# Optimization experiments

Hardware: AMD Instinct MI355X
Metric: run time of the kernel (lower is better)

## Reference

```python
import jax, jax.numpy as jnp
import numpy as np

B, N, DEG, F_IN, D = 32, 1024, 16, 8, 64

def setup_inputs() -> dict:
    key = jax.random.key(0)
    ks = jax.random.split(key, 24)
    T = B * N
    E = B * N * DEG
    x = jax.random.normal(ks[0], (T, F_IN), dtype=jnp.float32)
    # edges confined within each graph (block-diagonal batched graph)
    off = (jnp.arange(B) * N)[:, None]
    src = jax.random.randint(ks[1], (B, N * DEG), 0, N) + off
    dst = jax.random.randint(ks[2], (B, N * DEG), 0, N) + off
    edge_index = jnp.stack([src.reshape(-1), dst.reshape(-1)]).astype(jnp.int64)
    reachable = jax.random.randint(ks[3], (T,), 0, 2, dtype=jnp.int32)
    s = 0.1
    p = lambda k, shp: jax.random.normal(k, shp, dtype=jnp.float32) * s
    return {
        'x': x, 'edge_index': edge_index, 'reachable': reachable,
        'Wl0': p(ks[4], (D, F_IN)), 'Wr0': p(ks[5], (D, F_IN)),
        'att0': p(ks[6], (D,)), 'b0': p(ks[7], (D,)),
        'Wl': p(ks[8], (4, D, D)), 'Wr': p(ks[9], (4, D, D)),
        'att': p(ks[10], (4, D)), 'b': p(ks[11], (4, D)),
        't6w': p(ks[12], (D, D)), 't6b': p(ks[13], (D,)),
        't7w': p(ks[14], (D, D)), 't7b': p(ks[15], (D,)),
        't5pw': p(ks[16], (1, 2 * D)), 't5pb': p(ks[17], (1,)),
        't5vw': p(ks[18], (1, 2 * D)), 't5vb': p(ks[19], (1,)),
        'pw': p(ks[20], (1, 1)), 'pb': p(ks[21], (1,)),
        'vw': p(ks[22], (1, 1)), 'vb': p(ks[23], (1,)),
        'n_per_graph': N,
    }

def reference(x, edge_index, reachable, Wl0, Wr0, att0, b0, Wl, Wr, att, b,
              t6w, t6b, t7w, t7b, t5pw, t5pb, t5vw, t5vb, pw, pb, vw, vb,
              n_per_graph):
    T = x.shape[0]
    n = int(n_per_graph)
    bsz = T // n
    d = Wl0.shape[0]
    # GATv2Conv adds self loops by default
    loop = jnp.arange(T)
    src = jnp.concatenate([edge_index[0], loop])
    dst = jnp.concatenate([edge_index[1], loop])

    def gatv2(h, WlK, WrK, a, bb):
        xl = h @ WlK.T                                  # [T, d]
        xr = h @ WrK.T
        e = jax.nn.leaky_relu(xl[src] + xr[dst], 0.2) @ a  # [E]
        emax = jax.ops.segment_max(e, dst, num_segments=T)
        ee = jnp.exp(e - emax[dst])
        denom = jax.ops.segment_sum(ee, dst, num_segments=T)
        alpha = ee / denom[dst]                         # edge softmax per target
        return jax.ops.segment_sum(alpha[:, None] * xl[src], dst, num_segments=T) + bb

    h = gatv2(x, Wl0, Wr0, att0, b0)
    for k in range(Wl.shape[0]):  # ReLU between layers, none after last
        h = gatv2(jax.nn.relu(h), Wl[k], Wr[k], att[k], b[k])
    mu_raw = h                                          # [T, d]

    # scatter_mean pooling per graph + repeat_interleave back to nodes
    mu_mp = mu_raw.reshape(bsz, n, d).mean(axis=1)      # [B, d]
    mu_mp_exp = jnp.repeat(mu_mp, n, axis=0)            # [T, d]

    g = mu_mp_exp @ t6w.T + t6b
    l = mu_raw @ t7w.T + t7b
    rep = jax.nn.relu(jnp.concatenate([g, l], axis=1))  # [T, 2d]

    prob_logits = rep @ t5pw.T + t5pb                   # [T, 1]
    logits = (prob_logits * pw[0, 0] + pb[0]).reshape(bsz, n, 1)

    q = (rep @ t5vw.T + t5vb)[:, 0]                     # [T]
    q = jnp.where(reachable.astype(bool), q, jnp.float32(-1e20))
    v = q.reshape(bsz, n).max(axis=1, keepdims=True)    # [B, 1]
    value = v * vw[0, 0] + vb[0]
    return logits, value
```

## Files before the change

kernel.cpp:

```cpp
#include <hip/hip_runtime.h>
#include <hip/hip_bf16.h>

typedef unsigned short u16;

#define T_NODES 32768
#define NPG 1024
#define BGR 32
#define D 64
#define FIN 8
#define SLOTS 64

typedef __attribute__((ext_vector_type(8))) short short8v;
typedef __attribute__((ext_vector_type(4))) float floatx4;
typedef __attribute__((ext_vector_type(2))) float f32x2;

__device__ __forceinline__ float bf2f(u16 u){ return __uint_as_float(((unsigned)u) << 16); }
__device__ __forceinline__ u16 f2bf(float f){
    __hip_bfloat16 h = __float2bfloat16(f);
    return *reinterpret_cast<u16*>(&h);
}
__device__ __forceinline__ f32x2 lo_hi(unsigned w){
    f32x2 r;
    r[0] = __uint_as_float(w << 16);
    r[1] = __uint_as_float(w & 0xffff0000u);
    return r;
}
__device__ __forceinline__ f32x2 lrelu2(f32x2 v){
    return __builtin_elementwise_max(v, v * 0.2f);
}
__device__ __forceinline__ short8v pack_bf8(float4 a, float4 b){
    short8v r;
    r[0]=(short)f2bf(a.x); r[1]=(short)f2bf(a.y);
    r[2]=(short)f2bf(a.z); r[3]=(short)f2bf(a.w);
    r[4]=(short)f2bf(b.x); r[5]=(short)f2bf(b.y);
    r[6]=(short)f2bf(b.z); r[7]=(short)f2bf(b.w);
    return r;
}

__device__ __forceinline__ unsigned fenc(float f){
    unsigned b = __float_as_uint(f);
    return (b & 0x80000000u) ? ~b : (b | 0x80000000u);
}
__device__ __forceinline__ float fdec(unsigned k){
    unsigned b = (k & 0x80000000u) ? (k ^ 0x80000000u) : ~k;
    return __uint_as_float(b);
}

template<int CTRL, int RM, int BM>
__device__ __forceinline__ float dpp_add(float x){
    int y = __builtin_amdgcn_update_dpp(0, __float_as_int(x), CTRL, RM, BM, false);
    return x + __int_as_float(y);
}
__device__ __forceinline__ float wave_sum63(float x){
    x = dpp_add<0x111,0xf,0xf>(x);
    x = dpp_add<0x112,0xf,0xf>(x);
    x = dpp_add<0x114,0xf,0xe>(x);
    x = dpp_add<0x118,0xf,0xc>(x);
    x = dpp_add<0x142,0xa,0xf>(x);
    x = dpp_add<0x143,0xc,0xf>(x);
    return x;
}
__device__ __forceinline__ float wave_sum_bcast(float x){
    return __int_as_float(__builtin_amdgcn_readlane(__float_as_int(wave_sum63(x)), 63));
}
__device__ __forceinline__ float row_ror_add(float x){
    x = dpp_add<0x121,0xf,0xf>(x);
    x = dpp_add<0x122,0xf,0xf>(x);
    x = dpp_add<0x124,0xf,0xf>(x);
    x = dpp_add<0x128,0xf,0xf>(x);
    return x;
}

__device__ __forceinline__ void edge_body(uint2 uv, bool valid,
        f32x2 a01, f32x2 a23, f32x2 xr01, f32x2 xr23,
        f32x2& acc01, f32x2& acc23, float& l){
    f32x2 x01 = lo_hi(uv.x);
    f32x2 x23 = lo_hi(uv.y);
    f32x2 v01 = lrelu2(x01 + xr01);
    f32x2 v23 = lrelu2(x23 + xr23);
    f32x2 e2 = v01 * a01 + v23 * a23;
    float e = e2[0] + e2[1];
    e = row_ror_add(e);
    float q = valid ? __expf(e) : 0.f;
    acc01 += q * x01;
    acc23 += q * x23;
    l += q;
}

__device__ __forceinline__ void node_edge(const u16* __restrict__ xlin,
        const int* colSh, int eb, int t, int deg, int sub4,
        f32x2 a01, f32x2 a23, f32x2 xr01, f32x2 xr23,
        f32x2& acc01, f32x2& acc23, float& l){
    int nEdge = deg + 1;
    for (int j0 = 0; j0 < nEdge; j0 += 8){
        uint2 u[8];
        #pragma unroll
        for (int i = 0; i < 8; i++){
            int j = j0 + i;
            int jc = (j < nEdge) ? j : (nEdge-1);
            int s = (jc < deg) ? colSh[eb + jc] : t;
            u[i] = *(const uint2*)&xlin[((size_t)(unsigned)s << 6) + sub4];
        }
        #pragma unroll
        for (int i = 0; i < 8; i++)
            edge_body(u[i], j0 + i < nEdge, a01, a23, xr01, xr23, acc01, acc23, l);
    }
}

__global__ void countscat_kernel(const int* __restrict__ src, const int* __restrict__ dst,
                                 int* __restrict__ counts, int* __restrict__ col64, int E){
    int i = blockIdx.x*blockDim.x + threadIdx.x;
    if (i < E){
        int d = dst[i];
        int slot = atomicAdd(&counts[d], 1);
        if (slot < SLOTS) col64[((size_t)d << 6) + slot] = src[i];
    }
}

__global__ void lin0_kernel(const float* __restrict__ x, const float* __restrict__ Wl0,
                            const float* __restrict__ Wr0,
                            u16* __restrict__ xlb, u16* __restrict__ xrb,
                            int* __restrict__ counts, float* __restrict__ muAcc,
                            unsigned* __restrict__ vslot, int* __restrict__ done,
                            int* __restrict__ pgdone, int* __restrict__ pgflag){
    __shared__ float wl[D][FIN+1];
    __shared__ float wr[D][FIN+1];
    __shared__ float xs[32][FIN];
    int tid = threadIdx.x;
    int blk = blockIdx.x;
    int gidx = blk*256 + tid;
    if (gidx < T_NODES) counts[gidx] = 0;
    if (gidx < BGR*D)   muAcc[gidx] = 0.f;
    if (gidx < BGR){ vslot[gidx] = 0u; done[gidx] = 0; pgdone[gidx] = 0; pgflag[gidx] = 0; }
    int rowBase = (blk & 7)*4096 + (blk >> 3)*32;
    for (int i = tid; i < D*FIN; i += 256){
        wl[i>>3][i&7] = Wl0[i];
        wr[i>>3][i&7] = Wr0[i];
    }
    xs[tid>>3][tid&7] = x[rowBase*FIN + tid];
    __syncthreads();
    int wave = tid >> 6, lane = tid & 63;
    int rb = rowBase + wave*8;
    #pragma unroll
    for (int r = 0; r < 8; r++){
        float al = 0.f, ar = 0.f;
        int lr = wave*8 + r;
        #pragma unroll
        for (int k = 0; k < FIN; k++){
            float xv = xs[lr][k];
            al = fmaf(xv, wl[lane][k], al);
            ar = fmaf(xv, wr[lane][k], ar);
        }
        xlb[(size_t)(rb+r)*D + lane] = f2bf(al);
        xrb[(size_t)(rb+r)*D + lane] = f2bf(ar);
    }
}

__global__ __launch_bounds__(256) void el_kernel(
        const u16* __restrict__ xlin, const u16* __restrict__ xrin,
        const float* __restrict__ att, const float* __restrict__ bias,
        const int* __restrict__ counts, const int* __restrict__ col64,
        const float* __restrict__ Wl, const float* __restrict__ Wr,
        u16* __restrict__ xlout, u16* __restrict__ xrout){
    __shared__ __align__(16) u16 hs[16][80];
    __shared__ __align__(16) int colSh[16*SLOTS];
    __shared__ int cnt[16];
    int tid = threadIdx.x, blk = blockIdx.x;
    int rowBase = (blk & 7)*4096 + (blk >> 3)*16;
    if (tid < 16){
        int c = counts[rowBase + tid];
        cnt[tid] = c < SLOTS ? c : SLOTS;
    }
    *(int4*)&colSh[tid*4] = *(const int4*)&col64[((size_t)rowBase << 6) + tid*4];
    __syncthreads();
    int wave = tid >> 6, lane = tid & 63;
    int g = lane >> 4, sub4 = (lane & 15) << 2;
    int ln = wave*4 + g;
    int t  = rowBase + ln;
    f32x2 a01 = { att[sub4],   att[sub4+1] };
    f32x2 a23 = { att[sub4+2], att[sub4+3] };
    float4 b4 = *(const float4*)&bias[sub4];
    uint2 xru = *(const uint2*)&xrin[((size_t)t << 6) + sub4];
    f32x2 xr01 = lo_hi(xru.x), xr23 = lo_hi(xru.y);
    int deg = cnt[ln];
    f32x2 acc01 = {0.f,0.f}, acc23 = {0.f,0.f};
    float l = 0.f;
    node_edge(xlin, colSh, ln*SLOTS, t, deg, sub4,
              a01, a23, xr01, xr23, acc01, acc23, l);
    float rl = __frcp_rn(l);
    ushort4 hb;
    hb.x = f2bf(fmaxf(fmaf(acc01[0], rl, b4.x), 0.f));
    hb.y = f2bf(fmaxf(fmaf(acc01[1], rl, b4.y), 0.f));
    hb.z = f2bf(fmaxf(fmaf(acc23[0], rl, b4.z), 0.f));
    hb.w = f2bf(fmaxf(fmaf(acc23[1], rl, b4.w), 0.f));
    *(ushort4*)&hs[ln][sub4] = hb;
    int lw = lane & 15, lg = lane >> 4, kb = lg*8;
    int colw = (wave << 4) + lw;
    const float* wl0 = &Wl[colw*D + kb];
    const float* wr0 = &Wr[colw*D + kb];
    short8v bl0 = pack_bf8(*(const float4*)wl0,        *(const float4*)(wl0+4));
    short8v bl1 = pack_bf8(*(const float4*)(wl0+32),   *(const float4*)(wl0+36));
    short8v br0 = pack_bf8(*(const float4*)wr0,        *(const float4*)(wr0+4));
    short8v br1 = pack_bf8(*(const float4*)(wr0+32),   *(const float4*)(wr0+36));
    __syncthreads();
    short8v a0 = *(const short8v*)&hs[lw][kb];
    short8v a1 = *(const short8v*)&hs[lw][32 + kb];
    floatx4 cl = {0.f,0.f,0.f,0.f}, cr = {0.f,0.f,0.f,0.f};
    cl = __builtin_amdgcn_mfma_f32_16x16x32_bf16(a0, bl0, cl, 0, 0, 0);
    cl = __builtin_amdgcn_mfma_f32_16x16x32_bf16(a1, bl1, cl, 0, 0, 0);
    cr = __builtin_amdgcn_mfma_f32_16x16x32_bf16(a0, br0, cr, 0, 0, 0);
    cr = __builtin_amdgcn_mfma_f32_16x16x32_bf16(a1, br1, cr, 0, 0, 0);
    size_t rb = (size_t)(rowBase + lg*4);
    #pragma unroll
    for (int j = 0; j < 4; j++){
        xlout[(rb + j)*D + colw] = f2bf(cl[j]);
        xrout[(rb + j)*D + colw] = f2bf(cr[j]);
    }
}

__global__ __launch_bounds__(256) void e4final_kernel(
        const u16* __restrict__ xlin, const u16* __restrict__ xrin,
        const float* __restrict__ att, const float* __restrict__ bias,
        const int* __restrict__ counts, const int* __restrict__ col64,
        const float* __restrict__ t6w, const float* __restrict__ t6b,
        const float* __restrict__ t7w, const float* __restrict__ t7b,
        const float* __restrict__ t5pw, const float* __restrict__ t5pb,
        const float* __restrict__ t5vw, const float* __restrict__ t5vb,
        const float* __restrict__ pw, const float* __restrict__ pb,
        const float* __restrict__ vw, const float* __restrict__ vb,
        const int* __restrict__ reachable,
        float* __restrict__ muAcc, unsigned* __restrict__ vslot,
        int* __restrict__ done, int* __restrict__ pgdone,
        int* __restrict__ pgflag, float* __restrict__ gPQ,
        float* __restrict__ out_logits, float* __restrict__ out_value){
    __shared__ __align__(16) char arena[43776];
    __shared__ float muS[D];
    __shared__ float PgQgS[2];
    __shared__ int isLastS;
    float* hfin  = (float*)arena;
    int*   colSh = (int*)  (arena + 17408);
    int*   cnt   = (int*)  (arena + 33792);
    float* wsH   = (float*)(arena + 17408);
    float* ppar  = (float*)(arena + 34816);
    float* qpar  = (float*)(arena + 39168);

    int tid = threadIdx.x, blk = blockIdx.x;
    int rowBase = (blk & 7)*4096 + (blk >> 3)*64;
    int b = rowBase >> 10;
    if (tid < 64){
        int c = counts[rowBase + tid];
        cnt[tid] = c < SLOTS ? c : SLOTS;
    }
    for (int i = tid; i < 1024; i += 256)
        *(int4*)&colSh[i*4] = *(const int4*)&col64[((size_t)rowBase << 6) + i*4];
    __syncthreads();
    int wave = tid >> 6, lane = tid & 63;
    int g = lane >> 4, sub4 = (lane & 15) << 2;
    int gid = wave*4 + g;
    f32x2 a01 = { att[sub4],   att[sub4+1] };
    f32x2 a23 = { att[sub4+2], att[sub4+3] };
    float4 b4 = *(const float4*)&bias[sub4];
    for (int n = 0; n < 4; n++){
        int ln = gid + n*16;
        int t  = rowBase + ln;
        uint2 xru = *(const uint2*)&xrin[((size_t)t << 6) + sub4];
        f32x2 xr01 = lo_hi(xru.x), xr23 = lo_hi(xru.y);
        int deg = cnt[ln];
        f32x2 acc01 = {0.f,0.f}, acc23 = {0.f,0.f};
        float l = 0.f;
        node_edge(xlin, colSh, ln*SLOTS, t, deg, sub4,
                  a01, a23, xr01, xr23, acc01, acc23, l);
        float rl = __frcp_rn(l);
        float4 hv;
        hv.x = fmaf(acc01[0], rl, b4.x);
        hv.y = fmaf(acc01[1], rl, b4.y);
        hv.z = fmaf(acc23[0], rl, b4.z);
        hv.w = fmaf(acc23[1], rl, b4.w);
        *(float4*)&hfin[ln*68 + sub4] = hv;
    }
    __syncthreads();
    for (int i = tid; i < D*D; i += 256) wsH[(i>>6)*68 + (i&63)] = t7w[i];
    if (wave == 0){
        float s = 0.f;
        #pragma unroll
        for (int nn = 0; nn < 64; nn++) s += hfin[nn*68 + lane];
        atomicAdd(&muAcc[b*D + lane], s);
    }
    __syncthreads();
    if (tid == 0){
        int tk = atomicAdd(&pgdone[b], 1);
        isLastS = (tk == (NPG/64) - 1);
    }
    __syncthreads();
    if (isLastS){
        if (tid < D)
            muS[tid] = __hip_atomic_load(&muAcc[b*D + tid], __ATOMIC_RELAXED,
                                         __HIP_MEMORY_SCOPE_AGENT) * (1.f/NPG);
        __syncthreads();
        if (tid < D){
            int d = tid;
            float gg = t6b[d];
            #pragma unroll
            for (int k = 0; k < D; k++) gg = fmaf(muS[k], t6w[d*D + k], gg);
            gg = fmaxf(gg, 0.f);
            float pp = wave_sum_bcast(gg * t5pw[d]);
            float qq = wave_sum_bcast(gg * t5vw[d]);
            if (d == 0){
                __hip_atomic_store(&gPQ[b*2],   pp, __ATOMIC_RELAXED, __HIP_MEMORY_SCOPE_AGENT);
                __hip_atomic_store(&gPQ[b*2+1], qq, __ATOMIC_RELAXED, __HIP_MEMORY_SCOPE_AGENT);
                asm volatile("s_waitcnt vmcnt(0)" ::: "memory");
                __hip_atomic_store(&pgflag[b], 1, __ATOMIC_RELAXED, __HIP_MEMORY_SCOPE_AGENT);
            }
        }
    }
    int ty = tid >> 4, tx = tid & 15;
    int r0 = ty * 4;
    float acc[4][4];
    #pragma unroll
    for (int i = 0; i < 4; i++)
        #pragma unroll
        for (int j = 0; j < 4; j++) acc[i][j] = 0.f;
    for (int k = 0; k < D; k += 4){
        float4 hv[4], wv[4];
        #pragma unroll
        for (int i = 0; i < 4; i++){
            hv[i] = *(const float4*)&hfin[(r0+i)*68 + k];
            wv[i] = *(const float4*)&wsH[(tx + 16*i)*68 + k];
        }
        #pragma unroll
        for (int i = 0; i < 4; i++)
            #pragma unroll
            for (int j = 0; j < 4; j++)
                acc[i][j] += hv[i].x*wv[j].x + hv[i].y*wv[j].y
                           + hv[i].z*wv[j].z + hv[i].w*wv[j].w;
    }
    float bc[4], pwc[4], qwc[4];
    #pragma unroll
    for (int j = 0; j < 4; j++){
        int c = tx + 16*j;
        bc[j]  = t7b[c];
        pwc[j] = t5pw[D + c];
        qwc[j] = t5vw[D + c];
    }
    #pragma unroll
    for (int i = 0; i < 4; i++){
        float sp = 0.f, sq = 0.f;
        #pragma unroll
        for (int j = 0; j < 4; j++){
            float lv = fmaxf(acc[i][j] + bc[j], 0.f);
            sp = fmaf(lv, pwc[j], sp);
            sq = fmaf(lv, qwc[j], sq);
        }
        ppar[(r0+i)*17 + tx] = sp;
        qpar[(r0+i)*17 + tx] = sq;
    }
    __syncthreads();
    if (tid == 0){
        while (__hip_atomic_load(&pgflag[b], __ATOMIC_RELAXED,
                                 __HIP_MEMORY_SCOPE_AGENT) == 0)
            __builtin_amdgcn_s_sleep(16);
        PgQgS[0] = __hip_atomic_load(&gPQ[b*2],   __ATOMIC_RELAXED, __HIP_MEMORY_SCOPE_AGENT);
        PgQgS[1] = __hip_atomic_load(&gPQ[b*2+1], __ATOMIC_RELAXED, __HIP_MEMORY_SCOPE_AGENT);
    }
    __syncthreads();
    if (tid < 64){
        int t = rowBase + tid;
        float sp = 0.f, sq = 0.f;
        #pragma unroll
        for (int c = 0; c < 16; c++){ sp += ppar[tid*17 + c]; sq += qpar[tid*17 + c]; }
        float prob = PgQgS[0] + sp + t5pb[0];
        out_logits[t] = prob * pw[0] + pb[0];
        float q = PgQgS[1] + sq + t5vb[0];
        if (!reachable[t]) q = -1e20f;
        float m = q;
        #pragma unroll
        for (int o = 1; o < 64; o <<= 1) m = fmaxf(m, __shfl_xor(m, o, 64));
        if (tid == 0){
            atomicMax(&vslot[b], fenc(m));
            asm volatile("s_waitcnt vmcnt(0)" ::: "memory");
            int ticket = atomicAdd(&done[b], 1);
            if (ticket == (NPG/64) - 1){
                unsigned k = __hip_atomic_load(&vslot[b], __ATOMIC_RELAXED,
                                               __HIP_MEMORY_SCOPE_AGENT);
                out_value[b] = fdec(k)*vw[0] + vb[0];
            }
        }
    }
}

extern "C" void kernel_launch(void* const* d_in, const int* in_sizes, int n_in,
                              void* d_out, int out_size, void* d_ws, size_t ws_size,
                              hipStream_t stream){
    const float* x          = (const float*)d_in[0];
    const int*   edge_index = (const int*)d_in[1];
    const int*   reachable  = (const int*)d_in[2];
    const float* Wl0 = (const float*)d_in[3];
    const float* Wr0 = (const float*)d_in[4];
    const float* att0= (const float*)d_in[5];
    const float* b0  = (const float*)d_in[6];
    const float* Wl  = (const float*)d_in[7];
    const float* Wr  = (const float*)d_in[8];
    const float* att = (const float*)d_in[9];
    const float* bb  = (const float*)d_in[10];
    const float* t6w = (const float*)d_in[11];
    const float* t6b = (const float*)d_in[12];
    const float* t7w = (const float*)d_in[13];
    const float* t7b = (const float*)d_in[14];
    const float* t5pw= (const float*)d_in[15];
    const float* t5pb= (const float*)d_in[16];
    const float* t5vw= (const float*)d_in[17];
    const float* t5vb= (const float*)d_in[18];
    const float* pw  = (const float*)d_in[19];
    const float* pb  = (const float*)d_in[20];
    const float* vw  = (const float*)d_in[21];
    const float* vb  = (const float*)d_in[22];

    int E = in_sizes[1] / 2;
    const int* esrc = edge_index;
    const int* edst = edge_index + E;

    char* ws = (char*)d_ws;
    u16* xlbA   = (u16*)ws;
    u16* xrbA   = xlbA + (size_t)T_NODES*D;
    u16* xlbB   = xrbA + (size_t)T_NODES*D;
    u16* xrbB   = xlbB + (size_t)T_NODES*D;
    int* counts = (int*)(xrbB + (size_t)T_NODES*D);
    int* col64  = counts + T_NODES + 16;
    float* muAcc= (float*)(col64 + (size_t)T_NODES*SLOTS);
    unsigned* vslot = (unsigned*)(muAcc + BGR*D);
    int* done   = (int*)(vslot + BGR);
    int* pgdone = done + BGR;
    int* pgflag = pgdone + BGR;
    float* gPQ  = (float*)(pgflag + BGR);

    lin0_kernel<<<T_NODES/32, 256, 0, stream>>>(x, Wl0, Wr0, xlbA, xrbA,
                                                counts, muAcc, vslot, done,
                                                pgdone, pgflag);
    countscat_kernel<<<(E+255)/256, 256, 0, stream>>>(esrc, edst, counts, col64, E);

    el_kernel<<<T_NODES/16, 256, 0, stream>>>(xlbA, xrbA, att0, b0, counts, col64,
                                              Wl + 0*D*D, Wr + 0*D*D, xlbB, xrbB);
    el_kernel<<<T_NODES/16, 256, 0, stream>>>(xlbB, xrbB, att + 0*D, bb + 0*D, counts, col64,
                                              Wl + 1*D*D, Wr + 1*D*D, xlbA, xrbA);
    el_kernel<<<T_NODES/16, 256, 0, stream>>>(xlbA, xrbA, att + 1*D, bb + 1*D, counts, col64,
                                              Wl + 2*D*D, Wr + 2*D*D, xlbB, xrbB);
    el_kernel<<<T_NODES/16, 256, 0, stream>>>(xlbB, xrbB, att + 2*D, bb + 2*D, counts, col64,
                                              Wl + 3*D*D, Wr + 3*D*D, xlbA, xrbA);

    e4final_kernel<<<T_NODES/64, 256, 0, stream>>>(xlbA, xrbA, att + 3*D, bb + 3*D,
                                                   counts, col64, t6w, t6b, t7w, t7b,
                                                   t5pw, t5pb, t5vw, t5vb, pw, pb, vw, vb,
                                                   reachable, muAcc, vslot, done,
                                                   pgdone, pgflag, gPQ,
                                                   (float*)d_out, (float*)d_out + T_NODES);
}
```

Before: 233.6 us.

## Fuse edge bucketing into first GAT layer via grid barrier, double nodes per block

Removes the separate edge count/scatter kernel by folding it into the first layer kernel. Each of 1024 blocks scatters a slice of edges and then waits on a global atomic counter before running the attention step. All layer kernels now process 32 nodes per block instead of 16, halving the grid and reusing the packed weight fragments across two MFMA tiles. The spin barrier requires all 1024 blocks to be co-resident (launch bounds of 4 blocks per CU), otherwise it deadlocks. It also saves one launch and reduces block scheduling overhead.

```diff
diff --git a/kernel.cpp b/kernel.cpp
--- a/kernel.cpp
+++ b/kernel.cpp
@@ -9,6 +9,7 @@
 #define D 64
 #define FIN 8
 #define SLOTS 64
+#define NB_EL 1024
 
 typedef __attribute__((ext_vector_type(8))) short short8v;
 typedef __attribute__((ext_vector_type(4))) float floatx4;
@@ -107,13 +108,72 @@
     }
 }
 
-__global__ void countscat_kernel(const int* __restrict__ src, const int* __restrict__ dst,
-                                 int* __restrict__ counts, int* __restrict__ col64, int E){
-    int i = blockIdx.x*blockDim.x + threadIdx.x;
-    if (i < E){
-        int d = dst[i];
-        int slot = atomicAdd(&counts[d], 1);
-        if (slot < SLOTS) col64[((size_t)d << 6) + slot] = src[i];
+__device__ __forceinline__ void el_core(
+        const u16* __restrict__ xlin, const u16* __restrict__ xrin,
+        const float* __restrict__ att, const float* __restrict__ bias,
+        const int* __restrict__ counts, const int* __restrict__ col64,
+        const float* __restrict__ Wl, const float* __restrict__ Wr,
+        u16* __restrict__ xlout, u16* __restrict__ xrout,
+        int tid, int rowBase, u16 (*hs)[80], int* colSh, int* cnt){
+    if (tid < 32){
+        int c = counts[rowBase + tid];
+        cnt[tid] = c < SLOTS ? c : SLOTS;
+    }
+    #pragma unroll
+    for (int it = 0; it < 2; it++){
+        int i = it*256 + tid;
+        *(int4*)&colSh[i*4] = *(const int4*)&col64[((size_t)rowBase << 6) + i*4];
+    }
+    __syncthreads();
+    int wave = tid >> 6, lane = tid & 63;
+    int g = lane >> 4, sub4 = (lane & 15) << 2;
+    int gid = wave*4 + g;
+    f32x2 a01 = { att[sub4],   att[sub4+1] };
+    f32x2 a23 = { att[sub4+2], att[sub4+3] };
+    float4 b4 = *(const float4*)&bias[sub4];
+    #pragma unroll
+    for (int n = 0; n < 2; n++){
+        int ln = gid + n*16;
+        int t  = rowBase + ln;
+        uint2 xru = *(const uint2*)&xrin[((size_t)t << 6) + sub4];
+        f32x2 xr01 = lo_hi(xru.x), xr23 = lo_hi(xru.y);
+        int deg = cnt[ln];
+        f32x2 acc01 = {0.f,0.f}, acc23 = {0.f,0.f};
+        float l = 0.f;
+        node_edge(xlin, colSh, ln*SLOTS, t, deg, sub4,
+                  a01, a23, xr01, xr23, acc01, acc23, l);
+        float rl = __frcp_rn(l);
+        ushort4 hb;
+        hb.x = f2bf(fmaxf(fmaf(acc01[0], rl, b4.x), 0.f));
+        hb.y = f2bf(fmaxf(fmaf(acc01[1], rl, b4.y), 0.f));
+        hb.z = f2bf(fmaxf(fmaf(acc23[0], rl, b4.z), 0.f));
+        hb.w = f2bf(fmaxf(fmaf(acc23[1], rl, b4.w), 0.f));
+        *(ushort4*)&hs[ln][sub4] = hb;
+    }
+    int lw = lane & 15, lg = lane >> 4, kb = lg*8;
+    int colw = (wave << 4) + lw;
+    const float* wl0 = &Wl[colw*D + kb];
+    const float* wr0 = &Wr[colw*D + kb];
+    short8v bl0 = pack_bf8(*(const float4*)wl0,        *(const float4*)(wl0+4));
+    short8v bl1 = pack_bf8(*(const float4*)(wl0+32),   *(const float4*)(wl0+36));
+    short8v br0 = pack_bf8(*(const float4*)wr0,        *(const float4*)(wr0+4));
+    short8v br1 = pack_bf8(*(const float4*)(wr0+32),   *(const float4*)(wr0+36));
+    __syncthreads();
+    #pragma unroll
+    for (int mt = 0; mt < 2; mt++){
+        short8v a0 = *(const short8v*)&hs[mt*16 + lw][kb];
+        short8v a1 = *(const short8v*)&hs[mt*16 + lw][32 + kb];
+        floatx4 cl = {0.f,0.f,0.f,0.f}, cr = {0.f,0.f,0.f,0.f};
+        cl = __builtin_amdgcn_mfma_f32_16x16x32_bf16(a0, bl0, cl, 0, 0, 0);
+        cl = __builtin_amdgcn_mfma_f32_16x16x32_bf16(a1, bl1, cl, 0, 0, 0);
+        cr = __builtin_amdgcn_mfma_f32_16x16x32_bf16(a0, br0, cr, 0, 0, 0);
+        cr = __builtin_amdgcn_mfma_f32_16x16x32_bf16(a1, br1, cr, 0, 0, 0);
+        size_t rb = (size_t)(rowBase + mt*16 + lg*4);
+        #pragma unroll
+        for (int j = 0; j < 4; j++){
+            xlout[(rb + j)*D + colw] = f2bf(cl[j]);
+            xrout[(rb + j)*D + colw] = f2bf(cr[j]);
+        }
     }
 }
 
@@ -122,7 +182,8 @@
                             u16* __restrict__ xlb, u16* __restrict__ xrb,
                             int* __restrict__ counts, float* __restrict__ muAcc,
                             unsigned* __restrict__ vslot, int* __restrict__ done,
-                            int* __restrict__ pgdone, int* __restrict__ pgflag){
+                            int* __restrict__ pgdone, int* __restrict__ pgflag,
+                            int* __restrict__ zdone){
     __shared__ float wl[D][FIN+1];
     __shared__ float wr[D][FIN+1];
     __shared__ float xs[32][FIN];
@@ -132,6 +193,7 @@
     if (gidx < T_NODES) counts[gidx] = 0;
     if (gidx < BGR*D)   muAcc[gidx] = 0.f;
     if (gidx < BGR){ vslot[gidx] = 0u; done[gidx] = 0; pgdone[gidx] = 0; pgflag[gidx] = 0; }
+    if (gidx == 0) *zdone = 0;
     int rowBase = (blk & 7)*4096 + (blk >> 3)*32;
     for (int i = tid; i < D*FIN; i += 256){
         wl[i>>3][i&7] = Wl0[i];
@@ -154,6 +216,40 @@
         xlb[(size_t)(rb+r)*D + lane] = f2bf(al);
         xrb[(size_t)(rb+r)*D + lane] = f2bf(ar);
     }
+}
+
+__global__ __launch_bounds__(256, 4) void el_first(
+        const int* __restrict__ esrc, const int* __restrict__ edst, int E,
+        int* __restrict__ counts, int* __restrict__ col64, int* __restrict__ zdone,
+        const u16* __restrict__ xlin, const u16* __restrict__ xrin,
+        const float* __restrict__ att, const float* __restrict__ bias,
+        const float* __restrict__ Wl, const float* __restrict__ Wr,
+        u16* __restrict__ xlout, u16* __restrict__ xrout){
+    __shared__ __align__(16) u16 hs[32][80];
+    __shared__ __align__(16) int colSh[32*SLOTS];
+    __shared__ int cnt[32];
+    int tid = threadIdx.x, blk = blockIdx.x;
+    int rowBase = (blk & 7)*4096 + (blk >> 3)*32;
+    int per = (E + NB_EL - 1) / NB_EL;
+    int e0 = blk * per;
+    int e1 = e0 + per; e1 = e1 < E ? e1 : E;
+    for (int i = e0 + tid; i < e1; i += 256){
+        int d = edst[i];
+        int slot = atomicAdd(&counts[d], 1);
+        if (slot < SLOTS)
+            __hip_atomic_store(&col64[((size_t)d << 6) + slot], esrc[i],
+                               __ATOMIC_RELAXED, __HIP_MEMORY_SCOPE_AGENT);
+    }
+    __syncthreads();
+    if (tid == 0){
+        atomicAdd(zdone, 1);
+        while (__hip_atomic_load(zdone, __ATOMIC_RELAXED,
+                                 __HIP_MEMORY_SCOPE_AGENT) < NB_EL)
+            __builtin_amdgcn_s_sleep(32);
+    }
+    __syncthreads();
+    el_core(xlin, xrin, att, bias, counts, col64, Wl, Wr, xlout, xrout,
+            tid, rowBase, hs, colSh, cnt);
 }
 
 __global__ __launch_bounds__(256) void el_kernel(
@@ -162,60 +258,13 @@
         const int* __restrict__ counts, const int* __restrict__ col64,
         const float* __restrict__ Wl, const float* __restrict__ Wr,
         u16* __restrict__ xlout, u16* __restrict__ xrout){
-    __shared__ __align__(16) u16 hs[16][80];
-    __shared__ __align__(16) int colSh[16*SLOTS];
-    __shared__ int cnt[16];
+    __shared__ __align__(16) u16 hs[32][80];
+    __shared__ __align__(16) int colSh[32*SLOTS];
+    __shared__ int cnt[32];
     int tid = threadIdx.x, blk = blockIdx.x;
-    int rowBase = (blk & 7)*4096 + (blk >> 3)*16;
-    if (tid < 16){
-        int c = counts[rowBase + tid];
-        cnt[tid] = c < SLOTS ? c : SLOTS;
-    }
-    *(int4*)&colSh[tid*4] = *(const int4*)&col64[((size_t)rowBase << 6) + tid*4];
-    __syncthreads();
-    int wave = tid >> 6, lane = tid & 63;
-    int g = lane >> 4, sub4 = (lane & 15) << 2;
-    int ln = wave*4 + g;
-    int t  = rowBase + ln;
-    f32x2 a01 = { att[sub4],   att[sub4+1] };
-    f32x2 a23 = { att[sub4+2], att[sub4+3] };
-    float4 b4 = *(const float4*)&bias[sub4];
-    uint2 xru = *(const uint2*)&xrin[((size_t)t << 6) + sub4];
-    f32x2 xr01 = lo_hi(xru.x), xr23 = lo_hi(xru.y);
-    int deg = cnt[ln];
-    f32x2 acc01 = {0.f,0.f}, acc23 = {0.f,0.f};
-    float l = 0.f;
-    node_edge(xlin, colSh, ln*SLOTS, t, deg, sub4,
-              a01, a23, xr01, xr23, acc01, acc23, l);
-    float rl = __frcp_rn(l);
-    ushort4 hb;
-    hb.x = f2bf(fmaxf(fmaf(acc01[0], rl, b4.x), 0.f));
-    hb.y = f2bf(fmaxf(fmaf(acc01[1], rl, b4.y), 0.f));
-    hb.z = f2bf(fmaxf(fmaf(acc23[0], rl, b4.z), 0.f));
-    hb.w = f2bf(fmaxf(fmaf(acc23[1], rl, b4.w), 0.f));
-    *(ushort4*)&hs[ln][sub4] = hb;
-    int lw = lane & 15, lg = lane >> 4, kb = lg*8;
-    int colw = (wave << 4) + lw;
-    const float* wl0 = &Wl[colw*D + kb];
-    const float* wr0 = &Wr[colw*D + kb];
-    short8v bl0 = pack_bf8(*(const float4*)wl0,        *(const float4*)(wl0+4));
-    short8v bl1 = pack_bf8(*(const float4*)(wl0+32),   *(const float4*)(wl0+36));
-    short8v br0 = pack_bf8(*(const float4*)wr0,        *(const float4*)(wr0+4));
-    short8v br1 = pack_bf8(*(const float4*)(wr0+32),   *(const float4*)(wr0+36));
-    __syncthreads();
-    short8v a0 = *(const short8v*)&hs[lw][kb];
-    short8v a1 = *(const short8v*)&hs[lw][32 + kb];
-    floatx4 cl = {0.f,0.f,0.f,0.f}, cr = {0.f,0.f,0.f,0.f};
-    cl = __builtin_amdgcn_mfma_f32_16x16x32_bf16(a0, bl0, cl, 0, 0, 0);
-    cl = __builtin_amdgcn_mfma_f32_16x16x32_bf16(a1, bl1, cl, 0, 0, 0);
-    cr = __builtin_amdgcn_mfma_f32_16x16x32_bf16(a0, br0, cr, 0, 0, 0);
-    cr = __builtin_amdgcn_mfma_f32_16x16x32_bf16(a1, br1, cr, 0, 0, 0);
-    size_t rb = (size_t)(rowBase + lg*4);
-    #pragma unroll
-    for (int j = 0; j < 4; j++){
-        xlout[(rb + j)*D + colw] = f2bf(cl[j]);
-        xrout[(rb + j)*D + colw] = f2bf(cr[j]);
-    }
+    int rowBase = (blk & 7)*4096 + (blk >> 3)*32;
+    el_core(xlin, xrin, att, bias, counts, col64, Wl, Wr, xlout, xrout,
+            tid, rowBase, hs, colSh, cnt);
 }
 
 __global__ __launch_bounds__(256) void e4final_kernel(
@@ -432,20 +481,21 @@
     int* pgdone = done + BGR;
     int* pgflag = pgdone + BGR;
     float* gPQ  = (float*)(pgflag + BGR);
+    int* zdone  = (int*)(gPQ + 2*BGR);
 
     lin0_kernel<<<T_NODES/32, 256, 0, stream>>>(x, Wl0, Wr0, xlbA, xrbA,
                                                 counts, muAcc, vslot, done,
-                                                pgdone, pgflag);
-    countscat_kernel<<<(E+255)/256, 256, 0, stream>>>(esrc, edst, counts, col64, E);
-
-    el_kernel<<<T_NODES/16, 256, 0, stream>>>(xlbA, xrbA, att0, b0, counts, col64,
-                                              Wl + 0*D*D, Wr + 0*D*D, xlbB, xrbB);
-    el_kernel<<<T_NODES/16, 256, 0, stream>>>(xlbB, xrbB, att + 0*D, bb + 0*D, counts, col64,
-                                              Wl + 1*D*D, Wr + 1*D*D, xlbA, xrbA);
-    el_kernel<<<T_NODES/16, 256, 0, stream>>>(xlbA, xrbA, att + 1*D, bb + 1*D, counts, col64,
-                                              Wl + 2*D*D, Wr + 2*D*D, xlbB, xrbB);
-    el_kernel<<<T_NODES/16, 256, 0, stream>>>(xlbB, xrbB, att + 2*D, bb + 2*D, counts, col64,
-                                              Wl + 3*D*D, Wr + 3*D*D, xlbA, xrbA);
+                                                pgdone, pgflag, zdone);
+
+    el_first<<<NB_EL, 256, 0, stream>>>(esrc, edst, E, counts, col64, zdone,
+                                        xlbA, xrbA, att0, b0,
+                                        Wl + 0*D*D, Wr + 0*D*D, xlbB, xrbB);
+    el_kernel<<<NB_EL, 256, 0, stream>>>(xlbB, xrbB, att + 0*D, bb + 0*D, counts, col64,
+                                         Wl + 1*D*D, Wr + 1*D*D, xlbA, xrbA);
+    el_kernel<<<NB_EL, 256, 0, stream>>>(xlbA, xrbA, att + 1*D, bb + 1*D, counts, col64,
+                                         Wl + 2*D*D, Wr + 2*D*D, xlbB, xrbB);
+    el_kernel<<<NB_EL, 256, 0, stream>>>(xlbB, xrbB, att + 2*D, bb + 2*D, counts, col64,
+                                         Wl + 3*D*D, Wr + 3*D*D, xlbA, xrbA);
 
     e4final_kernel<<<T_NODES/64, 256, 0, stream>>>(xlbA, xrbA, att + 3*D, bb + 3*D,
                                                    counts, col64, t6w, t6b, t7w, t7b,
```

New measurement: 289.4 us. +23.9%, slower.

## Fuse edge bucketing into the first GAT layer via per-graph edge scan

Applied to the files above, without the earlier changes.

Removes the separate global-atomic countscat kernel. The first layer's kernel now builds each 16-node block's neighbor list in shared memory by scanning all edges of its graph with LDS atomics. It then writes counts and col64 out for the later layers. This drops a launch and the scattered global atomics, but every block redundantly rereads the whole graph's edge list, 64 times per graph. It also assumes edges are stored contiguously per graph.

```diff
diff --git a/kernel.cpp b/kernel.cpp
--- a/kernel.cpp
+++ b/kernel.cpp
@@ -107,72 +107,12 @@
     }
 }
 
-__global__ void countscat_kernel(const int* __restrict__ src, const int* __restrict__ dst,
-                                 int* __restrict__ counts, int* __restrict__ col64, int E){
-    int i = blockIdx.x*blockDim.x + threadIdx.x;
-    if (i < E){
-        int d = dst[i];
-        int slot = atomicAdd(&counts[d], 1);
-        if (slot < SLOTS) col64[((size_t)d << 6) + slot] = src[i];
-    }
-}
-
-__global__ void lin0_kernel(const float* __restrict__ x, const float* __restrict__ Wl0,
-                            const float* __restrict__ Wr0,
-                            u16* __restrict__ xlb, u16* __restrict__ xrb,
-                            int* __restrict__ counts, float* __restrict__ muAcc,
-                            unsigned* __restrict__ vslot, int* __restrict__ done,
-                            int* __restrict__ pgdone, int* __restrict__ pgflag){
-    __shared__ float wl[D][FIN+1];
-    __shared__ float wr[D][FIN+1];
-    __shared__ float xs[32][FIN];
-    int tid = threadIdx.x;
-    int blk = blockIdx.x;
-    int gidx = blk*256 + tid;
-    if (gidx < T_NODES) counts[gidx] = 0;
-    if (gidx < BGR*D)   muAcc[gidx] = 0.f;
-    if (gidx < BGR){ vslot[gidx] = 0u; done[gidx] = 0; pgdone[gidx] = 0; pgflag[gidx] = 0; }
-    int rowBase = (blk & 7)*4096 + (blk >> 3)*32;
-    for (int i = tid; i < D*FIN; i += 256){
-        wl[i>>3][i&7] = Wl0[i];
-        wr[i>>3][i&7] = Wr0[i];
-    }
-    xs[tid>>3][tid&7] = x[rowBase*FIN + tid];
-    __syncthreads();
-    int wave = tid >> 6, lane = tid & 63;
-    int rb = rowBase + wave*8;
-    #pragma unroll
-    for (int r = 0; r < 8; r++){
-        float al = 0.f, ar = 0.f;
-        int lr = wave*8 + r;
-        #pragma unroll
-        for (int k = 0; k < FIN; k++){
-            float xv = xs[lr][k];
-            al = fmaf(xv, wl[lane][k], al);
-            ar = fmaf(xv, wr[lane][k], ar);
-        }
-        xlb[(size_t)(rb+r)*D + lane] = f2bf(al);
-        xrb[(size_t)(rb+r)*D + lane] = f2bf(ar);
-    }
-}
-
-__global__ __launch_bounds__(256) void el_kernel(
+__device__ __forceinline__ void el_phase(
         const u16* __restrict__ xlin, const u16* __restrict__ xrin,
         const float* __restrict__ att, const float* __restrict__ bias,
-        const int* __restrict__ counts, const int* __restrict__ col64,
         const float* __restrict__ Wl, const float* __restrict__ Wr,
-        u16* __restrict__ xlout, u16* __restrict__ xrout){
-    __shared__ __align__(16) u16 hs[16][80];
-    __shared__ __align__(16) int colSh[16*SLOTS];
-    __shared__ int cnt[16];
-    int tid = threadIdx.x, blk = blockIdx.x;
-    int rowBase = (blk & 7)*4096 + (blk >> 3)*16;
-    if (tid < 16){
-        int c = counts[rowBase + tid];
-        cnt[tid] = c < SLOTS ? c : SLOTS;
-    }
-    *(int4*)&colSh[tid*4] = *(const int4*)&col64[((size_t)rowBase << 6) + tid*4];
-    __syncthreads();
+        u16* __restrict__ xlout, u16* __restrict__ xrout,
+        int tid, int rowBase, u16 (*hs)[80], const int* colSh, const int* cnt){
     int wave = tid >> 6, lane = tid & 63;
     int g = lane >> 4, sub4 = (lane & 15) << 2;
     int ln = wave*4 + g;
@@ -182,7 +122,7 @@
     float4 b4 = *(const float4*)&bias[sub4];
     uint2 xru = *(const uint2*)&xrin[((size_t)t << 6) + sub4];
     f32x2 xr01 = lo_hi(xru.x), xr23 = lo_hi(xru.y);
-    int deg = cnt[ln];
+    int deg = cnt[ln]; deg = deg < SLOTS ? deg : SLOTS;
     f32x2 acc01 = {0.f,0.f}, acc23 = {0.f,0.f};
     float l = 0.f;
     node_edge(xlin, colSh, ln*SLOTS, t, deg, sub4,
@@ -216,6 +156,97 @@
         xlout[(rb + j)*D + colw] = f2bf(cl[j]);
         xrout[(rb + j)*D + colw] = f2bf(cr[j]);
     }
+}
+
+__global__ void lin0_kernel(const float* __restrict__ x, const float* __restrict__ Wl0,
+                            const float* __restrict__ Wr0,
+                            u16* __restrict__ xlb, u16* __restrict__ xrb,
+                            float* __restrict__ muAcc,
+                            unsigned* __restrict__ vslot, int* __restrict__ done,
+                            int* __restrict__ pgdone, int* __restrict__ pgflag){
+    __shared__ float wl[D][FIN+1];
+    __shared__ float wr[D][FIN+1];
+    __shared__ float xs[32][FIN];
+    int tid = threadIdx.x;
+    int blk = blockIdx.x;
+    int gidx = blk*256 + tid;
+    if (gidx < BGR*D)   muAcc[gidx] = 0.f;
+    if (gidx < BGR){ vslot[gidx] = 0u; done[gidx] = 0; pgdone[gidx] = 0; pgflag[gidx] = 0; }
+    int rowBase = (blk & 7)*4096 + (blk >> 3)*32;
+    for (int i = tid; i < D*FIN; i += 256){
+        wl[i>>3][i&7] = Wl0[i];
+        wr[i>>3][i&7] = Wr0[i];
+    }
+    xs[tid>>3][tid&7] = x[rowBase*FIN + tid];
+    __syncthreads();
+    int wave = tid >> 6, lane = tid & 63;
+    int rb = rowBase + wave*8;
+    #pragma unroll
+    for (int r = 0; r < 8; r++){
+        float al = 0.f, ar = 0.f;
+        int lr = wave*8 + r;
+        #pragma unroll
+        for (int k = 0; k < FIN; k++){
+            float xv = xs[lr][k];
+            al = fmaf(xv, wl[lane][k], al);
+            ar = fmaf(xv, wr[lane][k], ar);
+        }
+        xlb[(size_t)(rb+r)*D + lane] = f2bf(al);
+        xrb[(size_t)(rb+r)*D + lane] = f2bf(ar);
+    }
+}
+
+__global__ __launch_bounds__(256) void el0_kernel(
+        const int* __restrict__ esrc, const int* __restrict__ edst, int epg,
+        const u16* __restrict__ xlin, const u16* __restrict__ xrin,
+        const float* __restrict__ att, const float* __restrict__ bias,
+        int* __restrict__ counts, int* __restrict__ col64,
+        const float* __restrict__ Wl, const float* __restrict__ Wr,
+        u16* __restrict__ xlout, u16* __restrict__ xrout){
+    __shared__ __align__(16) u16 hs[16][80];
+    __shared__ __align__(16) int colSh[16*SLOTS];
+    __shared__ int cntL[16];
+    int tid = threadIdx.x, blk = blockIdx.x;
+    int rowBase = (blk & 7)*4096 + (blk >> 3)*16;
+    int g = rowBase >> 10;
+    if (tid < 16) cntL[tid] = 0;
+    __syncthreads();
+    size_t eg0 = (size_t)g * epg;
+    const int4* d4 = (const int4*)(edst + eg0);
+    const int4* s4 = (const int4*)(esrc + eg0);
+    int q4 = epg >> 2;
+    for (int i = tid; i < q4; i += 256){
+        int4 dv = d4[i];
+        int4 sv = s4[i];
+        int r;
+        r = dv.x - rowBase; if ((unsigned)r < 16u){ int sl = atomicAdd(&cntL[r], 1); if (sl < SLOTS) colSh[(r<<6)+sl] = sv.x; }
+        r = dv.y - rowBase; if ((unsigned)r < 16u){ int sl = atomicAdd(&cntL[r], 1); if (sl < SLOTS) colSh[(r<<6)+sl] = sv.y; }
+        r = dv.z - rowBase; if ((unsigned)r < 16u){ int sl = atomicAdd(&cntL[r], 1); if (sl < SLOTS) colSh[(r<<6)+sl] = sv.z; }
+        r = dv.w - rowBase; if ((unsigned)r < 16u){ int sl = atomicAdd(&cntL[r], 1); if (sl < SLOTS) colSh[(r<<6)+sl] = sv.w; }
+    }
+    __syncthreads();
+    if (tid < 16) counts[rowBase + tid] = cntL[tid];
+    *(int4*)&col64[((size_t)rowBase << 6) + tid*4] = *(const int4*)&colSh[tid*4];
+    el_phase(xlin, xrin, att, bias, Wl, Wr, xlout, xrout,
+             tid, rowBase, hs, colSh, cntL);
+}
+
+__global__ __launch_bounds__(256) void el_kernel(
+        const u16* __restrict__ xlin, const u16* __restrict__ xrin,
+        const float* __restrict__ att, const float* __restrict__ bias,
+        const int* __restrict__ counts, const int* __restrict__ col64,
+        const float* __restrict__ Wl, const float* __restrict__ Wr,
+        u16* __restrict__ xlout, u16* __restrict__ xrout){
+    __shared__ __align__(16) u16 hs[16][80];
+    __shared__ __align__(16) int colSh[16*SLOTS];
+    __shared__ int cnt[16];
+    int tid = threadIdx.x, blk = blockIdx.x;
+    int rowBase = (blk & 7)*4096 + (blk >> 3)*16;
+    if (tid < 16) cnt[tid] = counts[rowBase + tid];
+    *(int4*)&colSh[tid*4] = *(const int4*)&col64[((size_t)rowBase << 6) + tid*4];
+    __syncthreads();
+    el_phase(xlin, xrin, att, bias, Wl, Wr, xlout, xrout,
+             tid, rowBase, hs, colSh, cnt);
 }
 
 __global__ __launch_bounds__(256) void e4final_kernel(
@@ -416,6 +447,7 @@
     const float* vb  = (const float*)d_in[22];
 
     int E = in_sizes[1] / 2;
+    int epg = E / BGR;
     const int* esrc = edge_index;
     const int* edst = edge_index + E;
 
@@ -434,12 +466,11 @@
     float* gPQ  = (float*)(pgflag + BGR);
 
     lin0_kernel<<<T_NODES/32, 256, 0, stream>>>(x, Wl0, Wr0, xlbA, xrbA,
-                                                counts, muAcc, vslot, done,
-                                                pgdone, pgflag);
-    countscat_kernel<<<(E+255)/256, 256, 0, stream>>>(esrc, edst, counts, col64, E);
-
-    el_kernel<<<T_NODES/16, 256, 0, stream>>>(xlbA, xrbA, att0, b0, counts, col64,
-                                              Wl + 0*D*D, Wr + 0*D*D, xlbB, xrbB);
+                                                muAcc, vslot, done, pgdone, pgflag);
+
+    el0_kernel<<<T_NODES/16, 256, 0, stream>>>(esrc, edst, epg, xlbA, xrbA, att0, b0,
+                                               counts, col64,
+                                               Wl + 0*D*D, Wr + 0*D*D, xlbB, xrbB);
     el_kernel<<<T_NODES/16, 256, 0, stream>>>(xlbB, xrbB, att + 0*D, bb + 0*D, counts, col64,
                                               Wl + 1*D*D, Wr + 1*D*D, xlbA, xrbA);
     el_kernel<<<T_NODES/16, 256, 0, stream>>>(xlbA, xrbA, att + 1*D, bb + 1*D, counts, col64,
```

Result: faster. 223.3 us (-4.4%).
